# Optimization experiments

Measured on AMD Instinct MI355X. Metric: run time of the kernel, lower is better.

## Reference

```python
import jax, jax.numpy as jnp
import numpy as np
from jax import lax

B, N, D = 8, 4096, 64
RATIO = 0.25
S = int(N * RATIO)  # 1024 sampled centroids
RADII = (0.1, 0.2, 0.4)
KS = (16, 32, 128)
MLPS = ((32, 32, 64), (64, 64, 128), (64, 96, 128))


def setup_inputs() -> dict:
    key = jax.random.key(0)
    ks = jax.random.split(key, 11)
    inp = {
        "xyz": jax.random.uniform(ks[0], (B, N, 3), dtype=jnp.float32),
        "features": jax.random.normal(ks[1], (B, N, D), dtype=jnp.float32),
    }
    c = 2
    for i, mlp in enumerate(MLPS):
        cin = D + 3  # in_channel + 3 prepended as in __init__
        for j, cout in enumerate(mlp):
            inp[f"w{i}_{j}"] = jax.random.normal(ks[c], (cout, cin), dtype=jnp.float32) * 0.02
            inp[f"b{i}_{j}"] = jnp.zeros((cout,), jnp.float32)
            c += 1
            cin = cout
    return inp


def fps(xyz, n_samples):
    # iterative farthest point sampling, vectorized over batch
    b, n, _ = xyz.shape

    def body(carry, _):
        dist, farthest = carry                                # [B,N], [B]
        centroid = xyz[jnp.arange(b), farthest]               # [B,3]
        d = jnp.sum((xyz - centroid[:, None, :]) ** 2, -1)    # [B,N]
        dist = jnp.minimum(dist, d)
        nxt = jnp.argmax(dist, -1).astype(jnp.int32)
        return (dist, nxt), farthest

    init = (jnp.full((b, n), 1e10, xyz.dtype), jnp.zeros((b,), jnp.int32))
    _, idxs = lax.scan(body, init, None, length=n_samples)    # [S,B]
    idxs = idxs.T                                             # [B,S]
    return jnp.take_along_axis(xyz, idxs[..., None], axis=1)  # [B,S,3]


def ball_group(xyz, new_xyz, features, radius, k):
    # ball query: up to k neighbors of each centroid within radius
    b, n, _ = xyz.shape
    s = new_xyz.shape[1]
    sqd = (jnp.sum(new_xyz ** 2, -1)[:, :, None]
           + jnp.sum(xyz ** 2, -1)[:, None, :]
           - 2.0 * jnp.einsum('bsc,bnc->bsn', new_xyz, xyz))   # [B,S,N]
    idx = jnp.broadcast_to(jnp.arange(n, dtype=jnp.int32), (b, s, n))
    idx = jnp.where(sqd > radius * radius, n, idx)
    idx = jnp.sort(idx, axis=-1)[:, :, :k]                     # [B,S,K]
    first = idx[:, :, :1]
    idx = jnp.where(idx == n, first, idx)                      # pad with first neighbor

    def gather(pts):
        return jnp.take_along_axis(pts, idx.reshape(b, s * k, 1), axis=1).reshape(b, s, k, pts.shape[-1])

    g_xyz = gather(xyz) - new_xyz[:, :, None, :]               # recentered offsets
    g_feat = gather(features)
    return jnp.concatenate([g_xyz, g_feat], axis=-1)           # [B,S,K,3+D]


def _forward(xyz, features, params):
    new_xyz = fps(xyz, S)
    outs = []
    for radius, k, layers in zip(RADII, KS, params):
        g = ball_group(xyz, new_xyz, features, radius, k)
        for w, bias in layers:  # 1x1 Conv2d == pointwise matmul, then ReLU
            g = jax.nn.relu(jnp.einsum('bskc,oc->bsko', g, w) + bias)
        outs.append(jnp.max(g, axis=2))                        # max-pool over K -> [B,S,Cout]
    return new_xyz, jnp.concatenate(outs, axis=-1)             # [B,S,3], [B,S,320]


def reference(xyz, features,
              w0_0, b0_0, w0_1, b0_1, w0_2, b0_2,
              w1_0, b1_0, w1_1, b1_1, w1_2, b1_2,
              w2_0, b2_0, w2_1, b2_1, w2_2, b2_2):
    params = [[(w0_0, b0_0), (w0_1, b0_1), (w0_2, b0_2)],
              [(w1_0, b1_0), (w1_1, b1_1), (w1_2, b1_2)],
              [(w2_0, b2_0), (w2_1, b2_1), (w2_2, b2_2)]]
    return _forward(xyz, features, params)
```

## Files before the change

### kernel.cpp

```cpp
#include <hip/hip_runtime.h>

#define NB   8
#define NPTS 4096
#define NS   1024
#define NF   64

typedef __bf16 bf16x8 __attribute__((ext_vector_type(8)));
typedef float  f32x4  __attribute__((ext_vector_type(4)));

struct WPrep {
  const float* src[9];
  int CO[9], CI[9], KC[9], off[9];
};

__global__ __launch_bounds__(256) void wprep_kernel(WPrep a, __bf16* __restrict__ dst) {
  const int id = blockIdx.y;
  const int t  = blockIdx.x * 256 + threadIdx.x;
  const int CT = a.CO[id] >> 4;
  const int KC = a.KC[id], CI = a.CI[id];
  if (t >= CT * KC * 64) return;
  const int lane = t & 63;
  const int fidx = t >> 6;
  const int kc = fidx % KC;
  const int ct = fidx / KC;
  const int n  = ct * 16 + (lane & 15);
  const int k0 = kc * 32 + (lane >> 4) * 8;
  const float* src = a.src[id];
  __bf16* d = dst + a.off[id] + (size_t)t * 8;
#pragma unroll
  for (int j = 0; j < 8; ++j) {
    const int k = k0 + j;
    d[j] = (__bf16)((k < CI) ? src[n * CI + k] : 0.0f);
  }
}

template <int CTRL>
__device__ __forceinline__ float dpp_fmax_step(float v) {
  const int t = __builtin_amdgcn_update_dpp(0, __float_as_int(v), CTRL, 0xf, 0xf, true);
  return fmaxf(v, __int_as_float(t));
}

__global__ __launch_bounds__(512) void fps_kernel(const float* __restrict__ xyz,
                                                  float* __restrict__ new_xyz) {
  const int b   = blockIdx.x;
  const int tid = threadIdx.x;
  __shared__ float sx[NPTS], sy[NPTS], sz[NPTS];
  __shared__ alignas(16) unsigned long long keys[16];

  const float* xb = xyz + (size_t)b * NPTS * 3;
  for (int p = tid; p < NPTS; p += 512) {
    sx[p] = xb[p * 3 + 0];
    sy[p] = xb[p * 3 + 1];
    sz[p] = xb[p * 3 + 2];
  }
  __syncthreads();

  float px[8], py[8], pz[8], dist[8];
#pragma unroll
  for (int r = 0; r < 8; ++r) {
    const int p = tid * 8 + r;
    px[r] = sx[p]; py[r] = sy[p]; pz[r] = sz[p];
    dist[r] = 1e10f;
  }

  const int wid  = tid >> 6;
  const int lane = tid & 63;
  int far = 0;
  for (int j = 0; j < NS; ++j) {
    const float cx = sx[far], cy = sy[far], cz = sz[far];
    if (tid == 0) {
      float* o = new_xyz + ((size_t)b * NS + j) * 3;
      o[0] = cx; o[1] = cy; o[2] = cz;
    }
    float bv = -1.0f;
    int   bi = 0;
#pragma unroll
    for (int r = 0; r < 8; ++r) {
      const float dx = __fsub_rn(px[r], cx);
      const float dy = __fsub_rn(py[r], cy);
      const float dz = __fsub_rn(pz[r], cz);
      const float d  = __fadd_rn(__fadd_rn(__fmul_rn(dx, dx), __fmul_rn(dy, dy)),
                                 __fmul_rn(dz, dz));
      const float nd = fminf(dist[r], d);
      dist[r] = nd;
      if (nd > bv) { bv = nd; bi = tid * 8 + r; }
    }
    float v = bv;
    v = dpp_fmax_step<0x111>(v);
    v = dpp_fmax_step<0x112>(v);
    v = dpp_fmax_step<0x114>(v);
    v = dpp_fmax_step<0x118>(v);
    v = dpp_fmax_step<0x142>(v);
    v = dpp_fmax_step<0x143>(v);
    const float wmax = __int_as_float(
        __builtin_amdgcn_readlane(__float_as_int(v), 63));
    const unsigned long long cand = __ballot(bv == wmax);
    const int fl = (int)__ffsll((long long)cand) - 1;
    const int par = (j & 1) * 8;
    if (lane == fl)
      keys[par + wid] = ((unsigned long long)__float_as_uint(wmax) << 32) |
                        (unsigned)(~bi);
    __syncthreads();
    const unsigned long long* kk = keys + par;
    unsigned long long k = kk[0];
#pragma unroll
    for (int i = 1; i < 8; ++i) {
      const unsigned long long o = kk[i];
      if (o > k) k = o;
    }
    far = (int)(~(unsigned)k) & 0xFFF;
  }
}

__global__ __launch_bounds__(64) void group_kernel(
    const float* __restrict__ xyz, const float* __restrict__ new_xyz,
    int* __restrict__ nbr0, int* __restrict__ nbr1, int* __restrict__ nbr2,
    int* __restrict__ cnt0, int* __restrict__ cnt1, int* __restrict__ cnt2) {
  const int bs   = blockIdx.x;
  const int b    = bs >> 10;
  const int lane = threadIdx.x;
  const float r2_0 = (float)(0.1 * 0.1);
  const float r2_1 = (float)(0.2 * 0.2);
  const float r2_2 = (float)(0.4 * 0.4);

  const float cx = new_xyz[bs * 3 + 0];
  const float cy = new_xyz[bs * 3 + 1];
  const float cz = new_xyz[bs * 3 + 2];
  const float sn = __fadd_rn(__fadd_rn(__fmul_rn(cx, cx), __fmul_rn(cy, cy)),
                             __fmul_rn(cz, cz));
  const float* xb = xyz + (size_t)b * NPTS * 3;
  const unsigned long long below = (1ull << lane) - 1ull;

  int c0 = 0, c1 = 0, c2 = 0;
  for (int base = 0; base < NPTS; base += 64) {
    const int p = base + lane;
    const float x = xb[p * 3 + 0], y = xb[p * 3 + 1], z = xb[p * 3 + 2];
    const float sp = __fadd_rn(__fadd_rn(__fmul_rn(x, x), __fmul_rn(y, y)),
                               __fmul_rn(z, z));
    const float dt = __fadd_rn(__fadd_rn(__fmul_rn(cx, x), __fmul_rn(cy, y)),
                               __fmul_rn(cz, z));
    const float sqd = __fsub_rn(__fadd_rn(sn, sp), __fmul_rn(2.0f, dt));
    const bool in0 = (sqd <= r2_0);
    const bool in1 = (sqd <= r2_1);
    const bool in2 = (sqd <= r2_2);
    const unsigned long long m0 = __ballot(in0);
    const unsigned long long m1 = __ballot(in1);
    const unsigned long long m2 = __ballot(in2);
    if (c0 < 16) {
      const int slot = c0 + __popcll(m0 & below);
      if (in0 && slot < 16) nbr0[bs * 16 + slot] = p;
      c0 = min(c0 + __popcll(m0), 16);
    }
    if (c1 < 32) {
      const int slot = c1 + __popcll(m1 & below);
      if (in1 && slot < 32) nbr1[bs * 32 + slot] = p;
      c1 = min(c1 + __popcll(m1), 32);
    }
    if (c2 < 128) {
      const int slot = c2 + __popcll(m2 & below);
      if (in2 && slot < 128) nbr2[bs * 128 + slot] = p;
      c2 = min(c2 + __popcll(m2), 128);
    }
    if (c0 == 16 && c1 == 32 && c2 == 128) break;
  }
  if (lane == 0) {
    cnt0[bs] = c0;
    cnt1[bs] = c1;
    cnt2[bs] = c2;
  }
}

template <int RT, int KC, int CO, int SIN, int SOUT, bool LAST>
__device__ __forceinline__ void wave_layer(const __bf16* in, __bf16* outb,
                                           const __bf16* __restrict__ wf,
                                           const float* __restrict__ bias,
                                           int lane, float* colmax) {
  bf16x8 a[RT][KC];
#pragma unroll
  for (int rt = 0; rt < RT; ++rt)
#pragma unroll
    for (int kc = 0; kc < KC; ++kc)
      a[rt][kc] = *(const bf16x8*)(in + (rt * 16 + (lane & 15)) * SIN + kc * 32 +
                                   (lane >> 4) * 8);
#pragma unroll
  for (int ct = 0; ct < CO / 16; ++ct) {
    const float bv = bias[ct * 16 + (lane & 15)];
    bf16x8 bfr[KC];
#pragma unroll
    for (int kc = 0; kc < KC; ++kc)
      bfr[kc] = *(const bf16x8*)(wf + ((size_t)(ct * KC + kc) * 64 + lane) * 8);
    float cm = 0.0f;
#pragma unroll
    for (int rt = 0; rt < RT; ++rt) {
      f32x4 acc = {0.0f, 0.0f, 0.0f, 0.0f};
#pragma unroll
      for (int kc = 0; kc < KC; ++kc)
        acc = __builtin_amdgcn_mfma_f32_16x16x32_bf16(a[rt][kc], bfr[kc], acc, 0, 0, 0);
      if constexpr (!LAST) {
#pragma unroll
        for (int r = 0; r < 4; ++r) {
          const int row = rt * 16 + (lane >> 4) * 4 + r;
          const float v = fmaxf(acc[r] + bv, 0.0f);
          outb[row * SOUT + ct * 16 + (lane & 15)] = (__bf16)v;
        }
      } else {
#pragma unroll
        for (int r = 0; r < 4; ++r) cm = fmaxf(cm, acc[r] + bv);
      }
    }
    if constexpr (LAST) colmax[ct] = fmaxf(colmax[ct], cm);
  }
}

template <int K, int C1, int C2, int C3, int WPP, int PPB>
__global__ __launch_bounds__(64 * WPP * PPB) void mlp_mfma(
    const float* __restrict__ xyz, const float* __restrict__ feat,
    const float* __restrict__ new_xyz,
    const int* __restrict__ nbr, const int* __restrict__ cnt_arr,
    const __bf16* __restrict__ wf1, const float* __restrict__ b1,
    const __bf16* __restrict__ wf2, const float* __restrict__ b2,
    const __bf16* __restrict__ wf3, const float* __restrict__ b3,
    float* __restrict__ out, int ch_off) {
  constexpr int SX  = 104;
  constexpr int SH1 = C1 + 8;
  constexpr int SH2 = C2 + 8;
  constexpr int KC1 = 3;
  constexpr int KC2 = C1 / 32;
  constexpr int KC3 = C2 / 32;
  constexpr int PT  = (104 + SH1) * K;
  constexpr int MW  = K / WPP;
  constexpr int RT  = MW / 16;
  static_assert(WPP == 1 || SH2 == SX, "h2 overlay must match X rows for WPP>1");
  __shared__ __bf16 lds[PPB * PT];
  __shared__ float  red[(WPP > 1) ? WPP * C3 : 1];

  const int tid  = threadIdx.x;
  const int lane = tid & 63;
  const int wid  = tid >> 6;

  constexpr int TPN = (64 * WPP) / K;
  constexpr int FPT = NF / TPN;
  {
    const int ln = tid / TPN;
    const int s  = tid - ln * TPN;
    const int lp = ln / K;
    const int n  = ln - lp * K;
    const int p  = blockIdx.x * PPB + lp;
    const int b  = p >> 10;
    const int cnt = cnt_arr[p];
    const int idx = nbr[p * K + min(n, cnt - 1)];
    __bf16* Xr = lds + lp * PT + n * SX;
    const float4* fp4 = (const float4*)(feat + ((size_t)b * NPTS + idx) * NF + s * FPT);
#pragma unroll
    for (int j = 0; j < FPT / 4; ++j) {
      const float4 v = fp4[j];
      Xr[3 + s * FPT + 4 * j + 0] = (__bf16)v.x;
      Xr[3 + s * FPT + 4 * j + 1] = (__bf16)v.y;
      Xr[3 + s * FPT + 4 * j + 2] = (__bf16)v.z;
      Xr[3 + s * FPT + 4 * j + 3] = (__bf16)v.w;
    }
    if (s == 0) {
      const float* xp = xyz + ((size_t)b * NPTS + idx) * 3;
      Xr[0] = (__bf16)(xp[0] - new_xyz[p * 3 + 0]);
      Xr[1] = (__bf16)(xp[1] - new_xyz[p * 3 + 1]);
      Xr[2] = (__bf16)(xp[2] - new_xyz[p * 3 + 2]);
#pragma unroll
      for (int k = 67; k < 96; ++k) Xr[k] = (__bf16)0.0f;
    }
  }

  const int lpg = wid / WPP;
  const int wv  = wid - lpg * WPP;
  const int p   = blockIdx.x * PPB + lpg;
  const __bf16* X  = lds + lpg * PT + wv * MW * SX;
  __bf16*       H1 = lds + lpg * PT + K * 104 + wv * MW * SH1;
  __bf16*       H2 = lds + lpg * PT + wv * MW * SH2;

  float colmax[C3 / 16];
#pragma unroll
  for (int ct = 0; ct < C3 / 16; ++ct) colmax[ct] = 0.0f;

  wave_layer<RT, KC1, C1, SX, SH1, false>(X, H1, wf1, b1, lane, nullptr);
  wave_layer<RT, KC2, C2, SH1, SH2, false>(H1, H2, wf2, b2, lane, nullptr);
  wave_layer<RT, KC3, C3, SH2, 0, true>(H2, nullptr, wf3, b3, lane, colmax);

#pragma unroll
  for (int ct = 0; ct < C3 / 16; ++ct) {
    float v = colmax[ct];
    v = fmaxf(v, __shfl_xor(v, 16));
    v = fmaxf(v, __shfl_xor(v, 32));
    colmax[ct] = v;
  }

  if constexpr (WPP == 1) {
    if (lane < 16) {
      float* op = out + (size_t)p * 320 + ch_off;
#pragma unroll
      for (int ct = 0; ct < C3 / 16; ++ct) op[ct * 16 + lane] = colmax[ct];
    }
  } else {
    if (lane < 16) {
#pragma unroll
      for (int ct = 0; ct < C3 / 16; ++ct)
        red[wv * C3 + ct * 16 + lane] = colmax[ct];
    }
    __syncthreads();
    if (tid < C3) {
      float v = red[tid];
#pragma unroll
      for (int w = 1; w < WPP; ++w) v = fmaxf(v, red[w * C3 + tid]);
      out[(size_t)p * 320 + ch_off + tid] = v;
    }
  }
}

extern "C" void kernel_launch(void* const* d_in, const int* in_sizes, int n_in,
                              void* d_out, int out_size, void* d_ws, size_t ws_size,
                              hipStream_t stream) {
  const float* xyz  = (const float*)d_in[0];
  const float* feat = (const float*)d_in[1];
  float* out      = (float*)d_out;
  float* new_xyz  = out;
  float* feat_out = out + 24576;

  __bf16* wsb = (__bf16*)d_ws;
  int*    wsi = (int*)d_ws;

  const int OW[9] = {0, 3072, 4096, 6144, 12288, 16384, 24576, 30720, 36864};
  const int widx[9] = {2, 4, 6, 8, 10, 12, 14, 16, 18};
  const int co[9] = {32, 32, 64, 64, 64, 128, 64, 96, 128};
  const int ci[9] = {67, 32, 32, 67, 64, 64, 67, 64, 96};
  const int kc[9] = {3, 1, 1, 3, 2, 2, 3, 2, 3};
  WPrep wp;
  for (int i = 0; i < 9; ++i) {
    wp.src[i] = (const float*)d_in[widx[i]];
    wp.CO[i] = co[i]; wp.CI[i] = ci[i]; wp.KC[i] = kc[i]; wp.off[i] = OW[i];
  }
  wprep_kernel<<<dim3(6, 9), 256, 0, stream>>>(wp, wsb);

  fps_kernel<<<NB, 512, 0, stream>>>(xyz, new_xyz);

  int* cnt0 = wsi + 24576;
  int* cnt1 = wsi + 32768;
  int* cnt2 = wsi + 40960;
  int* nbr0 = wsi + 49152;
  int* nbr1 = wsi + 180224;
  int* nbr2 = wsi + 442368;
  group_kernel<<<NB * NS, 64, 0, stream>>>(xyz, new_xyz, nbr0, nbr1, nbr2,
                                           cnt0, cnt1, cnt2);

  mlp_mfma<16, 32, 32, 64, 1, 4><<<NB * NS / 4, 256, 0, stream>>>(
      xyz, feat, new_xyz, nbr0, cnt0,
      wsb + OW[0], (const float*)d_in[3],
      wsb + OW[1], (const float*)d_in[5],
      wsb + OW[2], (const float*)d_in[7],
      feat_out, 0);
  mlp_mfma<32, 64, 64, 128, 1, 2><<<NB * NS / 2, 128, 0, stream>>>(
      xyz, feat, new_xyz, nbr1, cnt1,
      wsb + OW[3], (const float*)d_in[9],
      wsb + OW[4], (const float*)d_in[11],
      wsb + OW[5], (const float*)d_in[13],
      feat_out, 64);
  mlp_mfma<128, 64, 96, 128, 4, 1><<<NB * NS, 256, 0, stream>>>(
      xyz, feat, new_xyz, nbr2, cnt2,
      wsb + OW[6], (const float*)d_in[15],
      wsb + OW[7], (const float*)d_in[17],
      wsb + OW[8], (const float*)d_in[19],
      feat_out, 192);
}
```

Measured before the change: 893.1 us.

## Pack points as float4 with norms and shrink FPS block to four waves

Adds a prep kernel that packs xyz into float4 with the precomputed squared norm, so the grouping and MLP gather kernels do one aligned vector load per point instead of three strided scalar loads and recomputing the norm. The FPS kernel drops from 512 to 256 threads, with 16 points per thread and a 4-way cross-wave key reduction read as vector loads. The goal is less per-iteration barrier and reduction cost in the serial FPS loop. The trade-off is an extra kernel launch and longer per-thread work in FPS.

```diff
diff --git a/kernel.cpp b/kernel.cpp
--- a/kernel.cpp
+++ b/kernel.cpp
@@ -7,6 +7,7 @@
 
 typedef __bf16 bf16x8 __attribute__((ext_vector_type(8)));
 typedef float  f32x4  __attribute__((ext_vector_type(4)));
+typedef unsigned long long ullx2 __attribute__((ext_vector_type(2)));
 
 struct WPrep {
   const float* src[9];
@@ -34,31 +35,41 @@
   }
 }
 
+__global__ __launch_bounds__(256) void pts_prep(const float* __restrict__ xyz,
+                                                float4* __restrict__ pts4) {
+  const int i = blockIdx.x * 256 + threadIdx.x;
+  if (i >= NB * NPTS) return;
+  const float x = xyz[i * 3 + 0], y = xyz[i * 3 + 1], z = xyz[i * 3 + 2];
+  const float sp = __fadd_rn(__fadd_rn(__fmul_rn(x, x), __fmul_rn(y, y)),
+                             __fmul_rn(z, z));
+  pts4[i] = make_float4(x, y, z, sp);
+}
+
 template <int CTRL>
 __device__ __forceinline__ float dpp_fmax_step(float v) {
   const int t = __builtin_amdgcn_update_dpp(0, __float_as_int(v), CTRL, 0xf, 0xf, true);
   return fmaxf(v, __int_as_float(t));
 }
 
-__global__ __launch_bounds__(512) void fps_kernel(const float* __restrict__ xyz,
+__global__ __launch_bounds__(256) void fps_kernel(const float* __restrict__ xyz,
                                                   float* __restrict__ new_xyz) {
   const int b   = blockIdx.x;
   const int tid = threadIdx.x;
   __shared__ float sx[NPTS], sy[NPTS], sz[NPTS];
-  __shared__ alignas(16) unsigned long long keys[16];
+  __shared__ alignas(16) unsigned long long keys[8];
 
   const float* xb = xyz + (size_t)b * NPTS * 3;
-  for (int p = tid; p < NPTS; p += 512) {
+  for (int p = tid; p < NPTS; p += 256) {
     sx[p] = xb[p * 3 + 0];
     sy[p] = xb[p * 3 + 1];
     sz[p] = xb[p * 3 + 2];
   }
   __syncthreads();
 
-  float px[8], py[8], pz[8], dist[8];
-#pragma unroll
-  for (int r = 0; r < 8; ++r) {
-    const int p = tid * 8 + r;
+  float px[16], py[16], pz[16], dist[16];
+#pragma unroll
+  for (int r = 0; r < 16; ++r) {
+    const int p = tid * 16 + r;
     px[r] = sx[p]; py[r] = sy[p]; pz[r] = sz[p];
     dist[r] = 1e10f;
   }
@@ -75,7 +86,7 @@
     float bv = -1.0f;
     int   bi = 0;
 #pragma unroll
-    for (int r = 0; r < 8; ++r) {
+    for (int r = 0; r < 16; ++r) {
       const float dx = __fsub_rn(px[r], cx);
       const float dy = __fsub_rn(py[r], cy);
       const float dz = __fsub_rn(pz[r], cz);
@@ -83,7 +94,7 @@
                                  __fmul_rn(dz, dz));
       const float nd = fminf(dist[r], d);
       dist[r] = nd;
-      if (nd > bv) { bv = nd; bi = tid * 8 + r; }
+      if (nd > bv) { bv = nd; bi = tid * 16 + r; }
     }
     float v = bv;
     v = dpp_fmax_step<0x111>(v);
@@ -96,24 +107,23 @@
         __builtin_amdgcn_readlane(__float_as_int(v), 63));
     const unsigned long long cand = __ballot(bv == wmax);
     const int fl = (int)__ffsll((long long)cand) - 1;
-    const int par = (j & 1) * 8;
+    const int par = (j & 1) * 4;
     if (lane == fl)
       keys[par + wid] = ((unsigned long long)__float_as_uint(wmax) << 32) |
                         (unsigned)(~bi);
     __syncthreads();
-    const unsigned long long* kk = keys + par;
-    unsigned long long k = kk[0];
-#pragma unroll
-    for (int i = 1; i < 8; ++i) {
-      const unsigned long long o = kk[i];
-      if (o > k) k = o;
-    }
+    const ullx2 ka = *(const ullx2*)(keys + par);
+    const ullx2 kb = *(const ullx2*)(keys + par + 2);
+    unsigned long long k = ka.x;
+    if (ka.y > k) k = ka.y;
+    if (kb.x > k) k = kb.x;
+    if (kb.y > k) k = kb.y;
     far = (int)(~(unsigned)k) & 0xFFF;
   }
 }
 
 __global__ __launch_bounds__(64) void group_kernel(
-    const float* __restrict__ xyz, const float* __restrict__ new_xyz,
+    const float4* __restrict__ pts4, const float* __restrict__ new_xyz,
     int* __restrict__ nbr0, int* __restrict__ nbr1, int* __restrict__ nbr2,
     int* __restrict__ cnt0, int* __restrict__ cnt1, int* __restrict__ cnt2) {
   const int bs   = blockIdx.x;
@@ -128,18 +138,16 @@
   const float cz = new_xyz[bs * 3 + 2];
   const float sn = __fadd_rn(__fadd_rn(__fmul_rn(cx, cx), __fmul_rn(cy, cy)),
                              __fmul_rn(cz, cz));
-  const float* xb = xyz + (size_t)b * NPTS * 3;
+  const float4* pb = pts4 + (size_t)b * NPTS;
   const unsigned long long below = (1ull << lane) - 1ull;
 
   int c0 = 0, c1 = 0, c2 = 0;
   for (int base = 0; base < NPTS; base += 64) {
     const int p = base + lane;
-    const float x = xb[p * 3 + 0], y = xb[p * 3 + 1], z = xb[p * 3 + 2];
-    const float sp = __fadd_rn(__fadd_rn(__fmul_rn(x, x), __fmul_rn(y, y)),
-                               __fmul_rn(z, z));
-    const float dt = __fadd_rn(__fadd_rn(__fmul_rn(cx, x), __fmul_rn(cy, y)),
-                               __fmul_rn(cz, z));
-    const float sqd = __fsub_rn(__fadd_rn(sn, sp), __fmul_rn(2.0f, dt));
+    const float4 P = pb[p];
+    const float dt = __fadd_rn(__fadd_rn(__fmul_rn(cx, P.x), __fmul_rn(cy, P.y)),
+                               __fmul_rn(cz, P.z));
+    const float sqd = __fsub_rn(__fadd_rn(sn, P.w), __fmul_rn(2.0f, dt));
     const bool in0 = (sqd <= r2_0);
     const bool in1 = (sqd <= r2_1);
     const bool in2 = (sqd <= r2_2);
@@ -214,7 +222,7 @@
 
 template <int K, int C1, int C2, int C3, int WPP, int PPB>
 __global__ __launch_bounds__(64 * WPP * PPB) void mlp_mfma(
-    const float* __restrict__ xyz, const float* __restrict__ feat,
+    const float4* __restrict__ pts4, const float* __restrict__ feat,
     const float* __restrict__ new_xyz,
     const int* __restrict__ nbr, const int* __restrict__ cnt_arr,
     const __bf16* __restrict__ wf1, const float* __restrict__ b1,
@@ -260,10 +268,10 @@
       Xr[3 + s * FPT + 4 * j + 3] = (__bf16)v.w;
     }
     if (s == 0) {
-      const float* xp = xyz + ((size_t)b * NPTS + idx) * 3;
-      Xr[0] = (__bf16)(xp[0] - new_xyz[p * 3 + 0]);
-      Xr[1] = (__bf16)(xp[1] - new_xyz[p * 3 + 1]);
-      Xr[2] = (__bf16)(xp[2] - new_xyz[p * 3 + 2]);
+      const float4 P = pts4[(size_t)b * NPTS + idx];
+      Xr[0] = (__bf16)(P.x - new_xyz[p * 3 + 0]);
+      Xr[1] = (__bf16)(P.y - new_xyz[p * 3 + 1]);
+      Xr[2] = (__bf16)(P.z - new_xyz[p * 3 + 2]);
 #pragma unroll
       for (int k = 67; k < 96; ++k) Xr[k] = (__bf16)0.0f;
     }
@@ -338,7 +346,10 @@
   }
   wprep_kernel<<<dim3(6, 9), 256, 0, stream>>>(wp, wsb);
 
-  fps_kernel<<<NB, 512, 0, stream>>>(xyz, new_xyz);
+  float4* pts4 = (float4*)(wsi + 1490944);
+  pts_prep<<<(NB * NPTS + 255) / 256, 256, 0, stream>>>(xyz, pts4);
+
+  fps_kernel<<<NB, 256, 0, stream>>>(xyz, new_xyz);
 
   int* cnt0 = wsi + 24576;
   int* cnt1 = wsi + 32768;
@@ -346,23 +357,23 @@
   int* nbr0 = wsi + 49152;
   int* nbr1 = wsi + 180224;
   int* nbr2 = wsi + 442368;
-  group_kernel<<<NB * NS, 64, 0, stream>>>(xyz, new_xyz, nbr0, nbr1, nbr2,
+  group_kernel<<<NB * NS, 64, 0, stream>>>(pts4, new_xyz, nbr0, nbr1, nbr2,
                                            cnt0, cnt1, cnt2);
 
   mlp_mfma<16, 32, 32, 64, 1, 4><<<NB * NS / 4, 256, 0, stream>>>(
-      xyz, feat, new_xyz, nbr0, cnt0,
+      pts4, feat, new_xyz, nbr0, cnt0,
       wsb + OW[0], (const float*)d_in[3],
       wsb + OW[1], (const float*)d_in[5],
       wsb + OW[2], (const float*)d_in[7],
       feat_out, 0);
   mlp_mfma<32, 64, 64, 128, 1, 2><<<NB * NS / 2, 128, 0, stream>>>(
-      xyz, feat, new_xyz, nbr1, cnt1,
+      pts4, feat, new_xyz, nbr1, cnt1,
       wsb + OW[3], (const float*)d_in[9],
       wsb + OW[4], (const float*)d_in[11],
       wsb + OW[5], (const float*)d_in[13],
       feat_out, 64);
   mlp_mfma<128, 64, 96, 128, 4, 1><<<NB * NS, 256, 0, stream>>>(
-      xyz, feat, new_xyz, nbr2, cnt2,
+      pts4, feat, new_xyz, nbr2, cnt2,
       wsb + OW[6], (const float*)d_in[15],
       wsb + OW[7], (const float*)d_in[17],
       wsb + OW[8], (const float*)d_in[19],
```

Result: faster. 866.3 us (-3.0%).
